# Performance work log

Measured on AMD Instinct MI355X. Metric: run time of the kernel, lower is better.

Reference implementation:

```python
import jax, jax.numpy as jnp
import numpy as np

B, T, C, H = 4, 2048, 1024, 16
D = C // H  # head dim = 64

def precompute_rope(dim, max_pos):
    # rope_cache[t, i] = (cos(t*theta_i), sin(t*theta_i)), theta_i = 10000^(-2i/dim)
    i = jnp.arange(dim // 2, dtype=jnp.float32)
    theta = 1.0 / (10000.0 ** (2.0 * i / dim))
    t = jnp.arange(max_pos, dtype=jnp.float32)[:, None]
    ang = t * theta[None, :]
    return jnp.stack([jnp.cos(ang), jnp.sin(ang)], axis=-1)  # (max_pos, dim/2, 2)

def apply_rope(x, rope):
    # x: (B, H, T, D); complex multiply rope * x over pairs of channels
    Tq = x.shape[2]
    xr = x.reshape(x.shape[0], x.shape[1], Tq, D // 2, 2)
    a, b = xr[..., 0], xr[..., 1]
    c = rope[:Tq, :, 0]  # (T, D/2)
    s = rope[:Tq, :, 1]
    real = a * c - b * s
    imag = a * s + b * c
    return jnp.stack([real, imag], axis=-1).reshape(x.shape)

def setup_inputs() -> dict:
    key = jax.random.key(0)
    ks = jax.random.split(key, 9)
    scale = 1.0 / np.sqrt(C)
    def w(k):
        return jax.random.uniform(k, (C, C), jnp.float32, -scale, scale)
    def bvec(k):
        return jax.random.uniform(k, (C,), jnp.float32, -scale, scale)
    return {
        "x": jax.random.normal(ks[0], (B, T, C), jnp.float32),
        "Wq": w(ks[1]), "bq": bvec(ks[2]),
        "Wk": w(ks[3]), "bk": bvec(ks[4]),
        "Wv": w(ks[5]), "bv": bvec(ks[6]),
        "Wp": w(ks[7]), "bp": bvec(ks[8]),
        "rope_cache": precompute_rope(D, T),
    }

def reference(x, Wq, bq, Wk, bk, Wv, bv, Wp, bp, rope_cache):
    B_, T_, C_ = x.shape
    def heads(y):
        return y.reshape(B_, T_, H, D).transpose(0, 2, 1, 3)  # (B,H,T,D)
    q = heads(x @ Wq.T + bq)
    k = heads(x @ Wk.T + bk)
    v = heads(x @ Wv.T + bv)
    q = apply_rope(q, rope_cache)
    k = apply_rope(k, rope_cache)
    att = jnp.einsum("bhqd,bhkd->bhqk", q, k) * (1.0 / np.sqrt(D))
    causal = jnp.tril(jnp.ones((T_, T_), dtype=bool))
    att = jnp.where(causal, att, jnp.float32(-1e10))
    att = jax.nn.softmax(att, axis=-1)
    y = jnp.einsum("bhqk,bhkd->bhqd", att, v)
    y = y.transpose(0, 2, 1, 3).reshape(B_, T_, C_)
    return y @ Wp.T + bp
```

## Files before the change

### kernel.cpp

```cpp
#include <hip/hip_runtime.h>

#define DEVINL __device__ __forceinline__

typedef unsigned short u16;
typedef __attribute__((ext_vector_type(4))) short s16x4;
typedef __attribute__((ext_vector_type(8))) short s16x8;
typedef __attribute__((ext_vector_type(4))) float f32x4;

static constexpr int Bb = 4, Tt = 2048, Cc = 1024, Hh = 16, Dd = 64;
static constexpr int Mm = Bb * Tt;
static constexpr int KK = Cc;

DEVINL float bf2f(u16 u) { return __uint_as_float(((unsigned)u) << 16); }
DEVINL u16 f2bf(float f) {
  unsigned b = __float_as_uint(f);
  b += 0x7fff + ((b >> 16) & 1);
  return (u16)(b >> 16);
}
DEVINL unsigned cvtpk(float lo, float hi) {
  unsigned r;
  asm("v_cvt_pk_bf16_f32 %0, %1, %2" : "=v"(r) : "v"(lo), "v"(hi));
  return r;
}

#define GLDS(gsrc, ldst) \
  __builtin_amdgcn_global_load_lds((const __attribute__((address_space(1))) void*)(gsrc), \
                                   (__attribute__((address_space(3))) void*)(ldst), 16, 0, 0)

__global__ void cvt_bf16(const float* __restrict__ src, u16* __restrict__ dst, int n4) {
  int i = blockIdx.x * blockDim.x + threadIdx.x;
  int st = gridDim.x * blockDim.x;
  for (int g = i; g < n4; g += st) {
    float4 v = ((const float4*)src)[g];
    uint2 o;
    o.x = (unsigned)f2bf(v.x) | ((unsigned)f2bf(v.y) << 16);
    o.y = (unsigned)f2bf(v.z) | ((unsigned)f2bf(v.w) << 16);
    ((uint2*)dst)[g] = o;
  }
}

struct Cvt4Args { const float* s[4]; u16* d[4]; };
__global__ void cvt4(Cvt4Args a, int n4) {
  const float* __restrict__ src = a.s[blockIdx.y];
  u16* __restrict__ dst = a.d[blockIdx.y];
  int i = blockIdx.x * blockDim.x + threadIdx.x;
  int st = gridDim.x * blockDim.x;
  for (int g = i; g < n4; g += st) {
    float4 v = ((const float4*)src)[g];
    uint2 o;
    o.x = (unsigned)f2bf(v.x) | ((unsigned)f2bf(v.y) << 16);
    o.y = (unsigned)f2bf(v.z) | ((unsigned)f2bf(v.w) << 16);
    ((uint2*)dst)[g] = o;
  }
}

#define GEMM_PROLOG()                                              \
  const int tid = threadIdx.x, w = tid >> 6, l = tid & 63;         \
  const int lr = l & 15, lg = l >> 4;                              \
  const int m0 = blockIdx.x * 128, n0 = blockIdx.y * 128;          \
  const int wr = w >> 1, wc = w & 1;                               \
  f32x4 zero = {0.f, 0.f, 0.f, 0.f};                               \
  f32x4 acc[4][4];                                                 \
  _Pragma("unroll") for (int i = 0; i < 4; ++i)                    \
      _Pragma("unroll") for (int j = 0; j < 4; ++j) acc[i][j] = zero; \
  const int srow = l >> 3;                                         \
  const int scolsw = ((l & 7) ^ (l >> 3)) * 8;

#define GEMM_STAGE(Aptr, Wptr, k0, buf)                                                  \
  _Pragma("unroll") for (int i = 0; i < 4; ++i) {                                        \
    int row = i * 32 + w * 8 + srow;                                                     \
    GLDS(Aptr + (size_t)(m0 + row) * KK + (k0) + scolsw, &As[buf][(i * 32 + w * 8) * 64]); \
    GLDS(Wptr + (size_t)(n0 + row) * KK + (k0) + scolsw, &Bs[buf][(i * 32 + w * 8) * 64]); \
  }

#define GEMM_KLOOP_DB(Aptr, Wptr)                                                        \
  GEMM_STAGE(Aptr, Wptr, 0, 0)                                                           \
  for (int k0 = 0; k0 < KK; k0 += 64) {                                                  \
    const int buf = (k0 >> 6) & 1;                                                       \
    if (k0 + 64 < KK) {                                                                  \
      GEMM_STAGE(Aptr, Wptr, k0 + 64, buf ^ 1)                                           \
      asm volatile("s_waitcnt vmcnt(8)" ::: "memory");            \
    } else {                                                                             \
      asm volatile("s_waitcnt vmcnt(0)" ::: "memory");                                   \
    }                                                                                    \
    __builtin_amdgcn_s_barrier();                                                        \
    __builtin_amdgcn_sched_barrier(0);                                                   \
    _Pragma("unroll") for (int kk = 0; kk < 2; ++kk) {                                   \
      s16x8 af[4], bfr[4];                                                               \
      _Pragma("unroll") for (int i = 0; i < 4; ++i)                                      \
          af[i] = *(const s16x8*)&As[buf][(wr * 64 + i * 16 + lr) * 64 +                 \
                                         ((kk * 32 + lg * 8) ^ ((lr & 7) << 3))];        \
      _Pragma("unroll") for (int j = 0; j < 4; ++j)                                      \
          bfr[j] = *(const s16x8*)&Bs[buf][(wc * 64 + j * 16 + lr) * 64 +                \
                                          ((kk * 32 + lg * 8) ^ ((lr & 7) << 3))];       \
      _Pragma("unroll") for (int i = 0; i < 4; ++i)                                      \
          _Pragma("unroll") for (int j = 0; j < 4; ++j)                                  \
              acc[i][j] =                                                                \
                  __builtin_amdgcn_mfma_f32_16x16x32_bf16(af[i], bfr[j], acc[i][j], 0, 0, 0); \
    }                                                                                    \
    __builtin_amdgcn_sched_barrier(0);                                                   \
    __builtin_amdgcn_s_barrier();       \
  }

__global__ __launch_bounds__(256) void gemm_qk(const u16* __restrict__ A,
                                               const u16* __restrict__ W0,
                                               const u16* __restrict__ W1,
                                               const float* __restrict__ b0,
                                               const float* __restrict__ b1,
                                               const float* __restrict__ rope,
                                               u16* __restrict__ O0, u16* __restrict__ O1) {
  __shared__ __align__(16) u16 As[2][128 * 64];
  __shared__ __align__(16) u16 Bs[2][128 * 64];
  const int z = blockIdx.z;
  const u16* __restrict__ Wt = z ? W1 : W0;
  const float* __restrict__ bias = z ? b1 : b0;
  u16* __restrict__ O = z ? O1 : O0;
  const float scl = z ? 1.0f : 0.18033688f;
  GEMM_PROLOG()
  GEMM_KLOOP_DB(A, Wt)
#pragma unroll
  for (int j = 0; j < 4; ++j) {
    int ncol = n0 + wc * 64 + j * 16 + lr;
    float bj = bias[ncol];
    int hh = ncol >> 6, dd = ncol & 63;
    const float sign = (dd & 1) ? 1.0f : -1.0f;
    const float* csp = rope + (dd >> 1) * 2;
#pragma unroll
    for (int i = 0; i < 4; ++i) {
#pragma unroll
      for (int r = 0; r < 4; ++r) {
        int mrow = m0 + wr * 64 + i * 16 + lg * 4 + r;
        int bb2 = mrow >> 11, tt2 = mrow & (Tt - 1);
        float v = acc[i][j][r] + bj;
        float part = __shfl_xor(v, 1);
        float2 cs = *(const float2*)(csp + tt2 * 64);
        float outv = (v * cs.x + sign * part * cs.y) * scl;
        O[(((size_t)bb2 * Hh + hh) * Tt + tt2) * Dd + dd] = f2bf(outv);
      }
    }
  }
}

__global__ __launch_bounds__(256) void gemm_v(const u16* __restrict__ A,
                                              const u16* __restrict__ Wt,
                                              const float* __restrict__ bias,
                                              u16* __restrict__ O) {
  __shared__ __align__(16) u16 As[2][128 * 64];
  __shared__ __align__(16) u16 Bs[2][128 * 64];
  __shared__ __align__(16) u16 Ts[128 * 64];
  GEMM_PROLOG()
  GEMM_KLOOP_DB(A, Wt)
  const int bb2 = m0 >> 11, tloc = m0 & (Tt - 1);
#pragma unroll
  for (int p = 0; p < 2; ++p) {
    if (p) __syncthreads();
    if (wr == p) {
#pragma unroll
      for (int j = 0; j < 4; ++j) {
        int ncl = wc * 64 + j * 16 + lr;
        float bj = bias[n0 + ncl];
        int xw = (ncl & 3) << 2;
#pragma unroll
        for (int i = 0; i < 4; ++i) {
          s16x4 pk;
#pragma unroll
          for (int r = 0; r < 4; ++r) pk[r] = (short)f2bf(acc[i][j][r] + bj);
          *(s16x4*)&Ts[ncl * 64 + (((i * 4 + lg) ^ xw) << 2)] = pk;
        }
      }
    }
    __syncthreads();
    const int rn = tid >> 3, t8 = tid & 7;
#pragma unroll
    for (int it = 0; it < 4; ++it) {
      int rown = it * 32 + rn;
      int slot = (t8 * 2) ^ ((rown & 3) << 2);
      s16x8 v = *(const s16x8*)&Ts[rown * 64 + slot * 4];
      int ncol = n0 + rown;
      int hh2 = ncol >> 6, dd = ncol & 63;
      *(s16x8*)&O[(((size_t)bb2 * Hh + hh2) * Dd + dd) * Tt + tloc + p * 64 + t8 * 8] = v;
    }
  }
}

__global__ __launch_bounds__(256) void gemm_proj(const u16* __restrict__ A,
                                                 const u16* __restrict__ Wt,
                                                 const float* __restrict__ bias,
                                                 float* __restrict__ O) {
  __shared__ __align__(16) u16 As[2][128 * 64];
  __shared__ __align__(16) u16 Bs[2][128 * 64];
  GEMM_PROLOG()
  GEMM_KLOOP_DB(A, Wt)
#pragma unroll
  for (int j = 0; j < 4; ++j) {
    int ncol = n0 + wc * 64 + j * 16 + lr;
    float bj = bias[ncol];
#pragma unroll
    for (int i = 0; i < 4; ++i) {
#pragma unroll
      for (int r = 0; r < 4; ++r) {
        int mrow = m0 + wr * 64 + i * 16 + lg * 4 + r;
        O[(size_t)mrow * Cc + ncol] = acc[i][j][r] + bj;
      }
    }
  }
}

__global__ __launch_bounds__(256, 4) void attn_kernel(const u16* __restrict__ Q,
                                                      const u16* __restrict__ K,
                                                      const u16* __restrict__ VTg,
                                                      u16* __restrict__ Out) {
  __shared__ __align__(16) u16 Ks[2][64 * 64];
  __shared__ __align__(16) u16 VTs[2][64 * 64];
  __shared__ __align__(16) u16 Ps[4 * 16 * 32];
  const int tid = threadIdx.x, w = tid >> 6, l = tid & 63;
  const int lr = l & 15, lg = l >> 4;
  const int n = blockIdx.x + 16 * blockIdx.y;
  const int bh = ((n & 7) << 3) + (n >> 7);
  const int qpair = (n >> 3) & 15;
  const size_t base = (size_t)bh * Tt * Dd;
  const u16* Qp = Q + base;
  const u16* Kp = K + base;
  const u16* Vp = VTg + base;
  const int bb2 = bh >> 4, hh = bh & 15;
  const float NEG = -3.0e9f;
  f32x4 zero = {0.f, 0.f, 0.f, 0.f};
  const int krow_l = l >> 3, kc8sw = ((l & 7) ^ (l >> 3)) * 8;
  const int psw = (lr >> 1) & 3;

  auto process = [&](int qt) {
    const int qb0 = qt * 64;
    const int qrow = qb0 + w * 16 + lr;
    const int qg = qrow;
    s16x8 qf[2];
    qf[0] = *(const s16x8*)(Qp + (size_t)qrow * 64 + lg * 8);
    qf[1] = *(const s16x8*)(Qp + (size_t)qrow * 64 + 32 + lg * 8);
    f32x4 o[4] = {zero, zero, zero, zero};
    float m = -3e38f, lsum = 0.f;
    const int ktiles = qt + 1;
    auto stage = [&](int kt, int buf) {
      const int kk0 = kt * 64;
#pragma unroll
      for (int i = 0; i < 2; ++i) {
        int row = i * 32 + w * 8 + krow_l;
        GLDS(Kp + (size_t)(kk0 + row) * 64 + kc8sw, &Ks[buf][(i * 32 + w * 8) * 64]);
        GLDS(Vp + (size_t)row * Tt + kk0 + kc8sw, &VTs[buf][(i * 32 + w * 8) * 64]);
      }
    };
    stage(0, 0);
    for (int kt = 0; kt < ktiles; ++kt) {
      const int buf = kt & 1;
      if (kt + 1 < ktiles) {
        stage(kt + 1, buf ^ 1);
        asm volatile("s_waitcnt vmcnt(4)" ::: "memory");
      } else {
        asm volatile("s_waitcnt vmcnt(0)" ::: "memory");
      }
      __builtin_amdgcn_s_barrier();
      __builtin_amdgcn_sched_barrier(0);
      float pv[4][4];
      const int diag = (kt == ktiles - 1);
      __builtin_amdgcn_s_setprio(1);
#pragma unroll
      for (int cf = 0; cf < 4; ++cf) {
        f32x4 s = zero;
#pragma unroll
        for (int kf = 0; kf < 2; ++kf) {
          s16x8 kb = *(const s16x8*)&Ks[buf][(cf * 16 + lr) * 64 +
                                            (((kf * 4 + lg) ^ (lr & 7)) << 3)];
          s = __builtin_amdgcn_mfma_f32_16x16x32_bf16(kb, qf[kf], s, 0, 0, 0);
        }
        if (diag) {
          int key0 = kt * 64 + cf * 16 + lg * 4;
#pragma unroll
          for (int r = 0; r < 4; ++r) pv[cf][r] = (key0 + r <= qg) ? s[r] : NEG;
        } else {
#pragma unroll
          for (int r = 0; r < 4; ++r) pv[cf][r] = s[r];
        }
      }
      __builtin_amdgcn_s_setprio(0);
      float t0 = fmaxf(fmaxf(pv[0][0], pv[0][1]), fmaxf(pv[0][2], pv[0][3]));
#pragma unroll
      for (int cf = 1; cf < 4; ++cf) {
        float tc = fmaxf(fmaxf(pv[cf][0], pv[cf][1]), fmaxf(pv[cf][2], pv[cf][3]));
        t0 = fmaxf(t0, tc);
      }
      t0 = fmaxf(t0, __shfl_xor(t0, 16));
      float tm = fmaxf(t0, __shfl_xor(t0, 32));
      int stable = tm <= m + 11.5f;
      if (!__all(stable)) {
        float mn = fmaxf(m, tm);
        float fsc = __builtin_amdgcn_exp2f(m - mn);
        lsum *= fsc;
        m = mn;
#pragma unroll
        for (int jf = 0; jf < 4; ++jf) {
          o[jf][0] *= fsc; o[jf][1] *= fsc; o[jf][2] *= fsc; o[jf][3] *= fsc;
        }
      }
      float psum = 0.f;
#pragma unroll
      for (int cf = 0; cf < 4; ++cf)
#pragma unroll
        for (int r = 0; r < 4; ++r) {
          float p = __builtin_amdgcn_exp2f(pv[cf][r] - m);
          pv[cf][r] = p;
          psum += p;
        }
      psum += __shfl_xor(psum, 16);
      psum += __shfl_xor(psum, 32);
      lsum += psum;
#pragma unroll
      for (int kk = 0; kk < 2; ++kk) {
#pragma unroll
        for (int c = 0; c < 2; ++c) {
          int cf = kk * 2 + c;
          unsigned w0 = cvtpk(pv[cf][0], pv[cf][1]);
          unsigned w1 = cvtpk(pv[cf][2], pv[cf][3]);
          int col0 = c * 16 + lg * 4;
          int idx = w * 512 + lr * 32 + ((((col0 >> 3) ^ psw)) << 3) + (col0 & 7);
          *(unsigned*)&Ps[idx] = w0;
          *(unsigned*)&Ps[idx + 2] = w1;
        }
        s16x8 pa = *(const s16x8*)&Ps[w * 512 + lr * 32 + ((lg ^ psw) << 3)];
        __builtin_amdgcn_s_setprio(1);
#pragma unroll
        for (int jf = 0; jf < 4; ++jf) {
          s16x8 vb = *(const s16x8*)&VTs[buf][(jf * 16 + lr) * 64 +
                                             (((kk * 4 + lg) ^ (lr & 7)) << 3)];
          o[jf] = __builtin_amdgcn_mfma_f32_16x16x32_bf16(vb, pa, o[jf], 0, 0, 0);
        }
        __builtin_amdgcn_s_setprio(0);
      }
      __builtin_amdgcn_sched_barrier(0);
      __builtin_amdgcn_s_barrier();
    }
    float linv = 1.0f / lsum;
    int tq = qb0 + w * 16 + lr;
    u16* orow = Out + ((size_t)(bb2 * Tt + tq)) * Cc + hh * 64 + lg * 4;
#pragma unroll
    for (int jf = 0; jf < 4; ++jf) {
      uint2 pk;
      pk.x = cvtpk(o[jf][0] * linv, o[jf][1] * linv);
      pk.y = cvtpk(o[jf][2] * linv, o[jf][3] * linv);
      *(uint2*)&orow[jf * 16] = pk;
    }
  };

  process(qpair);
  process(31 - qpair);
}

extern "C" void kernel_launch(void* const* d_in, const int* in_sizes, int n_in,
                              void* d_out, int out_size, void* d_ws, size_t ws_size,
                              hipStream_t stream) {
  (void)in_sizes; (void)n_in; (void)out_size; (void)ws_size;
  const float* x = (const float*)d_in[0];
  const float* Wq = (const float*)d_in[1];
  const float* bq = (const float*)d_in[2];
  const float* Wk = (const float*)d_in[3];
  const float* bk = (const float*)d_in[4];
  const float* Wv = (const float*)d_in[5];
  const float* bv = (const float*)d_in[6];
  const float* Wp = (const float*)d_in[7];
  const float* bp = (const float*)d_in[8];
  const float* rope = (const float*)d_in[9];

  char* ws = (char*)d_ws;
  const size_t MB = 1024 * 1024;
  u16* xb  = (u16*)(ws + 0);
  u16* wqb = (u16*)(ws + 16 * MB);
  u16* wkb = (u16*)(ws + 18 * MB);
  u16* wvb = (u16*)(ws + 20 * MB);
  u16* wpb = (u16*)(ws + 22 * MB);
  u16* qb  = (u16*)(ws + 24 * MB);
  u16* kb  = (u16*)(ws + 40 * MB);
  u16* vt  = (u16*)(ws + 56 * MB);
  u16* att = (u16*)(ws + 72 * MB);

  cvt_bf16<<<2048, 256, 0, stream>>>(x, xb, (Mm * Cc) / 4);
  Cvt4Args ca;
  ca.s[0] = Wq; ca.s[1] = Wk; ca.s[2] = Wv; ca.s[3] = Wp;
  ca.d[0] = wqb; ca.d[1] = wkb; ca.d[2] = wvb; ca.d[3] = wpb;
  cvt4<<<dim3(256, 4), 256, 0, stream>>>(ca, (Cc * Cc) / 4);

  gemm_qk<<<dim3(Mm / 128, Cc / 128, 2), 256, 0, stream>>>(xb, wqb, wkb, bq, bk, rope, qb, kb);
  gemm_v<<<dim3(Mm / 128, Cc / 128), 256, 0, stream>>>(xb, wvb, bv, vt);

  attn_kernel<<<dim3(16, Bb * Hh), 256, 0, stream>>>(qb, kb, vt, att);

  gemm_proj<<<dim3(Mm / 128, Cc / 128), 256, 0, stream>>>(att, wpb, bp, (float*)d_out);
}
```

Measured before the change: 174.7 us.

## Process paired query tiles concurrently in 512-thread blocks sharing K/V tiles

The attention kernel now launches 512 threads per block. Waves 0-3 handle the high query tile and waves 4-7 the paired low tile, running at the same time instead of one after the other. Both halves share each staged K/V tile, so the low tile's K/V loads are no longer repeated and the serial second pass disappears. The low-tile waves sit idle through the later key tiles but still join every barrier. The per-tile row-sum shuffles move to the end, and the row-max shuffle now runs only on the rescale path. This relies on the block-wide __all vote staying valid across lanes.

```diff
diff --git a/kernel.cpp b/kernel.cpp
--- a/kernel.cpp
+++ b/kernel.cpp
@@ -206,18 +206,21 @@
   }
 }
 
-__global__ __launch_bounds__(256, 4) void attn_kernel(const u16* __restrict__ Q,
+__global__ __launch_bounds__(512, 8) void attn_kernel(const u16* __restrict__ Q,
                                                       const u16* __restrict__ K,
                                                       const u16* __restrict__ VTg,
                                                       u16* __restrict__ Out) {
   __shared__ __align__(16) u16 Ks[2][64 * 64];
   __shared__ __align__(16) u16 VTs[2][64 * 64];
-  __shared__ __align__(16) u16 Ps[4 * 16 * 32];
+  __shared__ __align__(16) u16 Ps[8 * 16 * 32];
   const int tid = threadIdx.x, w = tid >> 6, l = tid & 63;
   const int lr = l & 15, lg = l >> 4;
+  const int wq = w & 3;
   const int n = blockIdx.x + 16 * blockIdx.y;
   const int bh = ((n & 7) << 3) + (n >> 7);
-  const int qpair = (n >> 3) & 15;
+  const int qt = (n >> 3) & 15;
+  const int qtH = 31 - qt;
+  const int myqt = (w < 4) ? qtH : qt;
   const size_t base = (size_t)bh * Tt * Dd;
   const u16* Qp = Q + base;
   const u16* Kp = K + base;
@@ -228,38 +231,35 @@
   const int krow_l = l >> 3, kc8sw = ((l & 7) ^ (l >> 3)) * 8;
   const int psw = (lr >> 1) & 3;
 
-  auto process = [&](int qt) {
-    const int qb0 = qt * 64;
-    const int qrow = qb0 + w * 16 + lr;
-    const int qg = qrow;
-    s16x8 qf[2];
-    qf[0] = *(const s16x8*)(Qp + (size_t)qrow * 64 + lg * 8);
-    qf[1] = *(const s16x8*)(Qp + (size_t)qrow * 64 + 32 + lg * 8);
-    f32x4 o[4] = {zero, zero, zero, zero};
-    float m = -3e38f, lsum = 0.f;
-    const int ktiles = qt + 1;
-    auto stage = [&](int kt, int buf) {
-      const int kk0 = kt * 64;
-#pragma unroll
-      for (int i = 0; i < 2; ++i) {
-        int row = i * 32 + w * 8 + krow_l;
-        GLDS(Kp + (size_t)(kk0 + row) * 64 + kc8sw, &Ks[buf][(i * 32 + w * 8) * 64]);
-        GLDS(Vp + (size_t)row * Tt + kk0 + kc8sw, &VTs[buf][(i * 32 + w * 8) * 64]);
-      }
-    };
-    stage(0, 0);
-    for (int kt = 0; kt < ktiles; ++kt) {
-      const int buf = kt & 1;
-      if (kt + 1 < ktiles) {
-        stage(kt + 1, buf ^ 1);
-        asm volatile("s_waitcnt vmcnt(4)" ::: "memory");
-      } else {
-        asm volatile("s_waitcnt vmcnt(0)" ::: "memory");
-      }
-      __builtin_amdgcn_s_barrier();
-      __builtin_amdgcn_sched_barrier(0);
+  const int qg = myqt * 64 + wq * 16 + lr;
+  s16x8 qf[2];
+  qf[0] = *(const s16x8*)(Qp + (size_t)qg * 64 + lg * 8);
+  qf[1] = *(const s16x8*)(Qp + (size_t)qg * 64 + 32 + lg * 8);
+  f32x4 o[4] = {zero, zero, zero, zero};
+  float m = -3e38f, lsum = 0.f;
+
+  auto stage = [&](int kt, int buf) {
+    const int kk0 = kt * 64;
+    int row = w * 8 + krow_l;
+    GLDS(Kp + (size_t)(kk0 + row) * 64 + kc8sw, &Ks[buf][(w * 8) * 64]);
+    GLDS(Vp + (size_t)row * Tt + kk0 + kc8sw, &VTs[buf][(w * 8) * 64]);
+  };
+
+  const int htiles = qtH + 1;
+  stage(0, 0);
+  for (int kt = 0; kt < htiles; ++kt) {
+    const int buf = kt & 1;
+    if (kt + 1 < htiles) {
+      stage(kt + 1, buf ^ 1);
+      asm volatile("s_waitcnt vmcnt(2)" ::: "memory");
+    } else {
+      asm volatile("s_waitcnt vmcnt(0)" ::: "memory");
+    }
+    __builtin_amdgcn_s_barrier();
+    __builtin_amdgcn_sched_barrier(0);
+    if (w < 4 || kt <= qt) {
       float pv[4][4];
-      const int diag = (kt == ktiles - 1);
+      const int diag = (kt == myqt);
       __builtin_amdgcn_s_setprio(1);
 #pragma unroll
       for (int cf = 0; cf < 4; ++cf) {
@@ -286,10 +286,9 @@
         float tc = fmaxf(fmaxf(pv[cf][0], pv[cf][1]), fmaxf(pv[cf][2], pv[cf][3]));
         t0 = fmaxf(t0, tc);
       }
-      t0 = fmaxf(t0, __shfl_xor(t0, 16));
-      float tm = fmaxf(t0, __shfl_xor(t0, 32));
-      int stable = tm <= m + 11.5f;
-      if (!__all(stable)) {
+      if (!__all(t0 <= m + 11.5f)) {
+        float t1 = fmaxf(t0, __shfl_xor(t0, 16));
+        float tm = fmaxf(t1, __shfl_xor(t1, 32));
         float mn = fmaxf(m, tm);
         float fsc = __builtin_amdgcn_exp2f(m - mn);
         lsum *= fsc;
@@ -308,8 +307,6 @@
           pv[cf][r] = p;
           psum += p;
         }
-      psum += __shfl_xor(psum, 16);
-      psum += __shfl_xor(psum, 32);
       lsum += psum;
 #pragma unroll
       for (int kk = 0; kk < 2; ++kk) {
@@ -333,23 +330,21 @@
         }
         __builtin_amdgcn_s_setprio(0);
       }
-      __builtin_amdgcn_sched_barrier(0);
-      __builtin_amdgcn_s_barrier();
-    }
-    float linv = 1.0f / lsum;
-    int tq = qb0 + w * 16 + lr;
-    u16* orow = Out + ((size_t)(bb2 * Tt + tq)) * Cc + hh * 64 + lg * 4;
-#pragma unroll
-    for (int jf = 0; jf < 4; ++jf) {
-      uint2 pk;
-      pk.x = cvtpk(o[jf][0] * linv, o[jf][1] * linv);
-      pk.y = cvtpk(o[jf][2] * linv, o[jf][3] * linv);
-      *(uint2*)&orow[jf * 16] = pk;
-    }
-  };
-
-  process(qpair);
-  process(31 - qpair);
+    }
+    __builtin_amdgcn_sched_barrier(0);
+    __builtin_amdgcn_s_barrier();
+  }
+  lsum += __shfl_xor(lsum, 16);
+  lsum += __shfl_xor(lsum, 32);
+  float linv = 1.0f / lsum;
+  u16* orow = Out + ((size_t)(bb2 * Tt + qg)) * Cc + hh * 64 + lg * 4;
+#pragma unroll
+  for (int jf = 0; jf < 4; ++jf) {
+    uint2 pk;
+    pk.x = cvtpk(o[jf][0] * linv, o[jf][1] * linv);
+    pk.y = cvtpk(o[jf][2] * linv, o[jf][3] * linv);
+    *(uint2*)&orow[jf * 16] = pk;
+  }
 }
 
 extern "C" void kernel_launch(void* const* d_in, const int* in_sizes, int n_in,
@@ -388,7 +383,7 @@
   gemm_qk<<<dim3(Mm / 128, Cc / 128, 2), 256, 0, stream>>>(xb, wqb, wkb, bq, bk, rope, qb, kb);
   gemm_v<<<dim3(Mm / 128, Cc / 128), 256, 0, stream>>>(xb, wvb, bv, vt);
 
-  attn_kernel<<<dim3(16, Bb * Hh), 256, 0, stream>>>(qb, kb, vt, att);
+  attn_kernel<<<dim3(16, Bb * Hh), 512, 0, stream>>>(qb, kb, vt, att);
 
   gemm_proj<<<dim3(Mm / 128, Cc / 128), 256, 0, stream>>>(att, wpb, bp, (float*)d_out);
 }
```

New measurement: 178.2 us. 2.0% more time.
